# Optimization experiments

Hardware: AMD Instinct MI355X
Metric: run time of the kernel (lower is better)

## Reference

```python
import jax, jax.numpy as jnp
import numpy as np

DIM = 768
NUM_HEADS = 12
HEAD_DIM = DIM // NUM_HEADS
SCALE = HEAD_DIM ** -0.5


def setup_inputs() -> dict:
    key = jax.random.key(0)
    k1, k2, k3, k4 = jax.random.split(key, 4)
    B, N = 4, 2048
    x = jax.random.normal(k1, (B, N, DIM), dtype=jnp.float32)
    w_qkv = jax.random.normal(k2, (DIM, 3 * DIM), dtype=jnp.float32) * (DIM ** -0.5)
    w_proj = jax.random.normal(k3, (DIM, DIM), dtype=jnp.float32) * (DIM ** -0.5)
    b_proj = jax.random.normal(k4, (DIM,), dtype=jnp.float32) * 0.02
    return {"x": x, "w_qkv": w_qkv, "w_proj": w_proj, "b_proj": b_proj}


def reference(x, w_qkv, w_proj, b_proj):
    B, N, C = x.shape
    H, Dh = NUM_HEADS, HEAD_DIM
    # qkv: [B, N, 3, H, Dh] -> q,k,v each [B, H, N, Dh]
    qkv = (x @ w_qkv).reshape(B, N, 3, H, Dh)
    q = qkv[:, :, 0].transpose(0, 2, 1, 3) * SCALE
    k = qkv[:, :, 1].transpose(0, 2, 1, 3)
    v = qkv[:, :, 2].transpose(0, 2, 1, 3)
    attn = jax.nn.softmax(jnp.einsum('bhnd,bhmd->bhnm', q, k), axis=-1)
    out = jnp.einsum('bhnm,bhmd->bhnd', attn, v)  # [B, H, N, Dh]
    out = out.transpose(0, 2, 1, 3).reshape(B, N, C)
    return out @ w_proj + b_proj
```

## Files before the change

### kernel.cpp

```cpp
#include <hip/hip_runtime.h>

typedef unsigned short u16;
typedef __bf16 bf16x8 __attribute__((ext_vector_type(8)));
typedef float f32x4 __attribute__((ext_vector_type(4)));
typedef _Float16 f16x4 __attribute__((ext_vector_type(4)));
typedef unsigned short u16x8 __attribute__((ext_vector_type(8)));
typedef unsigned short u16x4 __attribute__((ext_vector_type(4)));

__device__ __forceinline__ u16 f2bf(float x) {
  union { float f; unsigned u; } c; c.f = x;
  unsigned r = c.u + 0x7FFFu + ((c.u >> 16) & 1u);
  return (u16)(r >> 16);
}

__device__ __forceinline__ void glds16(const void* g, void* s) {
  __builtin_amdgcn_global_load_lds(
      (const __attribute__((address_space(1))) unsigned int*)g,
      (__attribute__((address_space(3))) unsigned int*)s, 16, 0, 0);
}

__global__ __launch_bounds__(256) void k_pre(const float* __restrict__ x,
                                             u16* __restrict__ xbf,
                                             const float* __restrict__ wq,
                                             u16* __restrict__ wqt,
                                             const float* __restrict__ wp,
                                             u16* __restrict__ wpt) {
  __shared__ float tile[64 * 68];
  int bx = blockIdx.x;
  int tid = threadIdx.x;
  if (bx < 3072) {
    int i = bx * 256 + tid;
    const f32x4* xp = (const f32x4*)x + (size_t)i * 2;
    f32x4 a = xp[0], b = xp[1];
    u16x8 r;
    r[0] = f2bf(a[0]); r[1] = f2bf(a[1]); r[2] = f2bf(a[2]); r[3] = f2bf(a[3]);
    r[4] = f2bf(b[0]); r[5] = f2bf(b[1]); r[6] = f2bf(b[2]); r[7] = f2bf(b[3]);
    *((u16x8*)xbf + i) = r;
    return;
  }
  const float* src; u16* dst; int Nn, n0, k0;
  const int K = 768;
  if (bx < 3504) { int b2 = bx - 3072; src = wq; dst = wqt; Nn = 2304;
                   n0 = (b2 % 36) * 64; k0 = (b2 / 36) * 64; }
  else           { int b2 = bx - 3504; src = wp; dst = wpt; Nn = 768;
                   n0 = (b2 % 12) * 64; k0 = (b2 / 12) * 64; }
  int rr = tid >> 4, cc = tid & 15;
#pragma unroll
  for (int r = 0; r < 4; ++r) {
    int k = r * 16 + rr;
    f32x4 v = *(const f32x4*)(src + (size_t)(k0 + k) * Nn + n0 + cc * 4);
    *(f32x4*)(tile + k * 68 + cc * 4) = v;
  }
  __syncthreads();
#pragma unroll
  for (int r = 0; r < 4; ++r) {
    int n = r * 16 + rr;
    u16x4 o;
#pragma unroll
    for (int j = 0; j < 4; ++j) o[j] = f2bf(tile[(cc * 4 + j) * 68 + n]);
    *(u16x4*)(dst + (size_t)(n0 + n) * K + k0 + cc * 4) = o;
  }
}

template <int BM, int N, bool PROJ>
__global__ __launch_bounds__(256) void k_gemm(const u16* __restrict__ A,
                                              const u16* __restrict__ Bt,
                                              u16* __restrict__ Co,
                                              float* __restrict__ Cf,
                                              const float* __restrict__ bias,
                                              u16* __restrict__ vt) {
  const int K = 768;
  const int FI = BM / 32;
  __shared__ u16 lA[BM * 64];
  __shared__ u16 lB[128 * 64];
  const int tid = threadIdx.x;
  const int wave = tid >> 6, lane = tid & 63;
  const int lr = lane & 15, lq = lane >> 4;
  const int m0 = blockIdx.x * BM, n0 = blockIdx.y * 128;
  const int wr = (wave >> 1) * (BM / 2), wc = (wave & 1) * 64;
  f32x4 acc[FI][4] = {};
  for (int k0 = 0; k0 < K; k0 += 64) {
#pragma unroll
    for (int r = 0; r < BM / 32; ++r) {
      int ch = r * 256 + tid;
      int mm = ch >> 3, cs = ch & 7;
      glds16(A + (size_t)(m0 + mm) * K + k0 + ((cs ^ (mm & 7)) << 3), lA + ch * 8);
    }
#pragma unroll
    for (int r = 0; r < 4; ++r) {
      int ch = r * 256 + tid;
      int mm = ch >> 3, cs = ch & 7;
      glds16(Bt + (size_t)(n0 + mm) * K + k0 + ((cs ^ (mm & 7)) << 3), lB + ch * 8);
    }
    __syncthreads();
#pragma unroll
    for (int ks = 0; ks < 2; ++ks) {
      bf16x8 af[FI], bfr[4];
#pragma unroll
      for (int f = 0; f < FI; ++f) {
        int ma = wr + f * 16 + lr;
        af[f] = *(const bf16x8*)(lA + (ma * 8 + ((ks * 4 + lq) ^ (ma & 7))) * 8);
      }
#pragma unroll
      for (int f = 0; f < 4; ++f) {
        int nb = wc + f * 16 + lr;
        bfr[f] = *(const bf16x8*)(lB + (nb * 8 + ((ks * 4 + lq) ^ (nb & 7))) * 8);
      }
#pragma unroll
      for (int fi = 0; fi < FI; ++fi)
#pragma unroll
        for (int fj = 0; fj < 4; ++fj)
          acc[fi][fj] = __builtin_amdgcn_mfma_f32_16x16x32_bf16(
              af[fi], bfr[fj], acc[fi][fj], 0, 0, 0);
    }
    __syncthreads();
  }
#pragma unroll
  for (int fi = 0; fi < FI; ++fi) {
#pragma unroll
    for (int fj = 0; fj < 4; ++fj) {
      int row = m0 + wr + fi * 16 + lq * 4;
      int col = n0 + wc + fj * 16 + lr;
      if constexpr (PROJ) {
        float bv = bias[col];
#pragma unroll
        for (int g = 0; g < 4; ++g)
          Cf[(size_t)(row + g) * N + col] = acc[fi][fj][g] + bv;
      } else {
        if (n0 + wc >= 1536) {
          int hh = (col - 1536) >> 6, dd = col & 63;
          int sl = row & 2047;
          int g4 = (sl >> 2) & 31;
          int p = ((g4 >> 3) << 3) | ((g4 & 3) << 1) | ((g4 >> 2) & 1);
          int seqp = (sl & ~127) | (p << 2);
          u16x4 o;
#pragma unroll
          for (int g = 0; g < 4; ++g) o[g] = f2bf(acc[fi][fj][g]);
          *(u16x4*)(vt + (((size_t)(row >> 11) * 12 + hh) * 64 + dd) * 2048 +
                    seqp) = o;
        } else {
          const float qs = 0.18033688011112042f;
          float s = (col < 768) ? qs : 1.0f;
#pragma unroll
          for (int g = 0; g < 4; ++g)
            Co[(size_t)(row + g) * N + col] = f2bf(acc[fi][fj][g] * s);
        }
      }
    }
  }
}

__global__ __launch_bounds__(256, 2) void k_attn(const u16* __restrict__ qkv,
                                                 const u16* __restrict__ vt,
                                                 u16* __restrict__ p0,
                                                 u16* __restrict__ p1,
                                                 float* __restrict__ Lp) {
  const int SEQ = 2048, C3 = 2304;
  __shared__ u16 lds[32768];
  const int tid = threadIdx.x;
  const int wave = tid >> 6, lane = tid & 63;
  const int lr = lane & 15, lq = lane >> 4;
  const int n0 = blockIdx.x * 256;
  const int bh = blockIdx.y;
  const int jh = blockIdx.z;
  const int b = bh / 12, h = bh % 12;
  const u16* qb = qkv + (size_t)b * SEQ * C3 + h * 64;
  const u16* kb = qb + 768;
  const u16* vb = vt + (size_t)bh * 64 * SEQ;

#pragma unroll
  for (int r = 0; r < 8; ++r) {
    int ch = r * 256 + tid;
    int mm = ch >> 3, cs = ch & 7;
    glds16(qb + (size_t)(n0 + mm) * C3 + ((cs ^ (mm & 7)) << 3), lds + ch * 8);
  }
  __syncthreads();
  bf16x8 qf[4][2];
#pragma unroll
  for (int rf = 0; rf < 4; ++rf) {
    int mq = wave * 64 + rf * 16 + lr;
#pragma unroll
    for (int ks = 0; ks < 2; ++ks)
      qf[rf][ks] = *(const bf16x8*)(lds + (mq * 8 + ((ks * 4 + lq) ^ (mq & 7))) * 8);
  }
  __syncthreads();

  const f32x4 biasC = {-8.f, -8.f, -8.f, -8.f};
  union { u16x8 u; bf16x8 b; } onesU;
#pragma unroll
  for (int e = 0; e < 8; ++e) onesU.u[e] = 0x3F80;
  const bf16x8 onesA = onesU.b;
  f32x4 O[4][4] = {};
  f32x4 L5[4] = {};

  auto stage = [&](int t, int buf) {
    int j0 = jh * 1024 + t * 128;
    u16* K_ = lds + buf * 8192;
    u16* V_ = lds + 16384 + buf * 8192;
#pragma unroll
    for (int r = 0; r < 4; ++r) {
      int ch = r * 256 + tid;
      int mm = ch >> 3, cs = ch & 7;
      glds16(kb + (size_t)(j0 + mm) * C3 + ((cs ^ (mm & 7)) << 3), K_ + ch * 8);
    }
#pragma unroll
    for (int r = 0; r < 4; ++r) {
      int ch = r * 256 + tid;
      int dd = ch >> 4, ct = ch & 15;
      glds16(vb + (size_t)dd * SEQ + j0 + ((ct ^ (dd & 7)) << 3), V_ + ch * 8);
    }
  };

  stage(0, 0);
  for (int t = 0; t < 8; ++t) {
    const int cur = t & 1;
    const u16* K_ = lds + cur * 8192;
    const u16* V_ = lds + 16384 + cur * 8192;
    asm volatile("s_barrier" ::: "memory");
    if (t < 7) {
      stage(t + 1, cur ^ 1);
      asm volatile("s_waitcnt vmcnt(8)" ::: "memory");
    } else {
      asm volatile("s_waitcnt vmcnt(0)" ::: "memory");
    }
    asm volatile("s_barrier" ::: "memory");

#pragma unroll
    for (int c = 0; c < 4; ++c) {
      f32x4 S[2][4];
#pragma unroll
      for (int j2 = 0; j2 < 2; ++j2) {
        int j = (c * 2 + j2) * 16 + lr;
        bf16x8 kf = *(const bf16x8*)(K_ + (j * 8 + (lq ^ (j & 7))) * 8);
#pragma unroll
        for (int rf = 0; rf < 4; ++rf)
          S[j2][rf] = __builtin_amdgcn_mfma_f32_16x16x32_bf16(
              kf, qf[rf][0], biasC, 0, 0, 0);
      }
#pragma unroll
      for (int j2 = 0; j2 < 2; ++j2) {
        int j = (c * 2 + j2) * 16 + lr;
        bf16x8 kf = *(const bf16x8*)(K_ + (j * 8 + ((4 + lq) ^ (j & 7))) * 8);
#pragma unroll
        for (int rf = 0; rf < 4; ++rf)
          S[j2][rf] = __builtin_amdgcn_mfma_f32_16x16x32_bf16(
              kf, qf[rf][1], S[j2][rf], 0, 0, 0);
      }
      bf16x8 P[4];
#pragma unroll
      for (int rf = 0; rf < 4; ++rf) {
        bf16x8 p8;
#pragma unroll
        for (int j2 = 0; j2 < 2; ++j2)
#pragma unroll
          for (int g = 0; g < 4; ++g)
            p8[j2 * 4 + g] = (__bf16)__builtin_amdgcn_exp2f(S[j2][rf][g]);
        P[rf] = p8;
        L5[rf] = __builtin_amdgcn_mfma_f32_16x16x32_bf16(
            onesA, P[rf], L5[rf], 0, 0, 0);
      }
#pragma unroll
      for (int df = 0; df < 4; ++df) {
        int d = df * 16 + lr;
        bf16x8 vf = *(const bf16x8*)(V_ + d * 128 + (((c * 4 + lq) ^ (d & 7)) << 3));
#pragma unroll
        for (int rf = 0; rf < 4; ++rf)
          O[rf][df] = __builtin_amdgcn_mfma_f32_16x16x32_bf16(
              vf, P[rf], O[rf][df], 0, 0, 0);
      }
    }
  }

  u16* pd = jh ? p1 : p0;
  float* Lb = Lp + (size_t)(jh * 48 + bh) * 2048;
#pragma unroll
  for (int rf = 0; rf < 4; ++rf) {
    int rowl = n0 + wave * 64 + rf * 16 + lr;
    if (lq == 0) Lb[rowl] = L5[rf][0];
    size_t row = (size_t)b * SEQ + rowl;
#pragma unroll
    for (int df = 0; df < 4; ++df) {
      union { f16x4 h; u16x4 u; } o;
#pragma unroll
      for (int g = 0; g < 4; ++g) o.h[g] = (_Float16)O[rf][df][g];
      *(u16x4*)(pd + row * 768 + h * 64 + df * 16 + lq * 4) = o.u;
    }
  }
}

__global__ __launch_bounds__(256) void k_merge(const u16* __restrict__ p0,
                                               u16* __restrict__ p1,
                                               const float* __restrict__ Lp) {
  int t = blockIdx.x * 256 + threadIdx.x;
  int row = t / 192, c4 = (t % 192) * 4;
  int hh = c4 >> 6;
  int bh = (row >> 11) * 12 + hh, rowl = row & 2047;
  float l = Lp[(size_t)bh * 2048 + rowl] + Lp[(size_t)(48 + bh) * 2048 + rowl];
  float inv = 1.0f / l;
  size_t off = (size_t)row * 768 + c4;
  union { f16x4 h; u16x4 u; } a, bb;
  a.u = *(const u16x4*)(p0 + off);
  bb.u = *(const u16x4*)(p1 + off);
  u16x4 o;
#pragma unroll
  for (int g = 0; g < 4; ++g)
    o[g] = f2bf(((float)a.h[g] + (float)bb.h[g]) * inv);
  *(u16x4*)(p1 + off) = o;
}

extern "C" void kernel_launch(void* const* d_in, const int* in_sizes, int n_in,
                              void* d_out, int out_size, void* d_ws, size_t ws_size,
                              hipStream_t stream) {
  const float* x = (const float*)d_in[0];
  const float* w_qkv = (const float*)d_in[1];
  const float* w_proj = (const float*)d_in[2];
  const float* b_proj = (const float*)d_in[3];
  float* out = (float*)d_out;
  char* ws = (char*)d_ws;
  u16* x_bf    = (u16*)(ws);
  u16* wqkv_t  = (u16*)(ws + 12582912);
  u16* wproj_t = (u16*)(ws + 16121856);
  u16* qkv     = (u16*)(ws + 17301504);
  u16* vt      = (u16*)(ws + 55050240);
  u16* aout    = (u16*)(ws + 67633152);
  float* Lp    = (float*)wqkv_t;

  k_pre<<<3648, 256, 0, stream>>>(x, x_bf, w_qkv, wqkv_t, w_proj, wproj_t);
  k_gemm<128, 2304, false><<<dim3(64, 18), 256, 0, stream>>>(x_bf, wqkv_t, qkv,
                                                             nullptr, nullptr, vt);
  k_attn<<<dim3(8, 48, 2), 256, 0, stream>>>(qkv, vt, x_bf, aout, Lp);
  k_merge<<<6144, 256, 0, stream>>>(x_bf, aout, Lp);
  k_gemm<64, 768, true><<<dim3(128, 6), 256, 0, stream>>>(aout, wproj_t, nullptr,
                                                          out, b_proj, nullptr);
}
```

Baseline: 215.9 us.

## Double-buffer GEMM K-loop and single-buffer V in attention for higher occupancy

The QKV/proj GEMM kernel now walks K in 32-wide steps with double-buffered LDS, issuing the next tile's async global-to-LDS loads while the current tile runs MFMAs, and declares 4 blocks per CU. The attention kernel keeps K double-buffered but gives V a single buffer, loaded each iteration and waited on only after the first QK chunk. This cuts attention LDS enough to target 3 blocks per CU. The aim is better latency hiding and occupancy, at the cost of more barriers per K-step and a tighter register budget under the new launch bounds.

```diff
diff --git a/kernel.cpp b/kernel.cpp
--- a/kernel.cpp
+++ b/kernel.cpp
@@ -63,58 +63,78 @@
 }
 
 template <int BM, int N, bool PROJ>
-__global__ __launch_bounds__(256) void k_gemm(const u16* __restrict__ A,
-                                              const u16* __restrict__ Bt,
-                                              u16* __restrict__ Co,
-                                              float* __restrict__ Cf,
-                                              const float* __restrict__ bias,
-                                              u16* __restrict__ vt) {
+__global__ __launch_bounds__(256, 4) void k_gemm(const u16* __restrict__ A,
+                                                 const u16* __restrict__ Bt,
+                                                 u16* __restrict__ Co,
+                                                 float* __restrict__ Cf,
+                                                 const float* __restrict__ bias,
+                                                 u16* __restrict__ vt) {
   const int K = 768;
   const int FI = BM / 32;
-  __shared__ u16 lA[BM * 64];
-  __shared__ u16 lB[128 * 64];
+  __shared__ u16 lds[2 * (BM + 128) * 32];
   const int tid = threadIdx.x;
   const int wave = tid >> 6, lane = tid & 63;
   const int lr = lane & 15, lq = lane >> 4;
   const int m0 = blockIdx.x * BM, n0 = blockIdx.y * 128;
   const int wr = (wave >> 1) * (BM / 2), wc = (wave & 1) * 64;
   f32x4 acc[FI][4] = {};
-  for (int k0 = 0; k0 < K; k0 += 64) {
-#pragma unroll
-    for (int r = 0; r < BM / 32; ++r) {
+
+  auto stage = [&](int t, int buf) {
+    int k0 = t * 32;
+    u16* sA = lds + buf * ((BM + 128) * 32);
+    u16* sB = sA + BM * 32;
+#pragma unroll
+    for (int r = 0; r < BM / 64; ++r) {
       int ch = r * 256 + tid;
-      int mm = ch >> 3, cs = ch & 7;
-      glds16(A + (size_t)(m0 + mm) * K + k0 + ((cs ^ (mm & 7)) << 3), lA + ch * 8);
-    }
-#pragma unroll
-    for (int r = 0; r < 4; ++r) {
+      int mm = ch >> 2, cs = ch & 3;
+      glds16(A + (size_t)(m0 + mm) * K + k0 + ((cs ^ ((mm >> 1) & 3)) << 3),
+             sA + ch * 8);
+    }
+#pragma unroll
+    for (int r = 0; r < 2; ++r) {
       int ch = r * 256 + tid;
-      int mm = ch >> 3, cs = ch & 7;
-      glds16(Bt + (size_t)(n0 + mm) * K + k0 + ((cs ^ (mm & 7)) << 3), lB + ch * 8);
-    }
-    __syncthreads();
-#pragma unroll
-    for (int ks = 0; ks < 2; ++ks) {
-      bf16x8 af[FI], bfr[4];
-#pragma unroll
-      for (int f = 0; f < FI; ++f) {
-        int ma = wr + f * 16 + lr;
-        af[f] = *(const bf16x8*)(lA + (ma * 8 + ((ks * 4 + lq) ^ (ma & 7))) * 8);
-      }
-#pragma unroll
-      for (int f = 0; f < 4; ++f) {
-        int nb = wc + f * 16 + lr;
-        bfr[f] = *(const bf16x8*)(lB + (nb * 8 + ((ks * 4 + lq) ^ (nb & 7))) * 8);
-      }
-#pragma unroll
-      for (int fi = 0; fi < FI; ++fi)
-#pragma unroll
-        for (int fj = 0; fj < 4; ++fj)
-          acc[fi][fj] = __builtin_amdgcn_mfma_f32_16x16x32_bf16(
-              af[fi], bfr[fj], acc[fi][fj], 0, 0, 0);
-    }
-    __syncthreads();
-  }
+      int mm = ch >> 2, cs = ch & 3;
+      glds16(Bt + (size_t)(n0 + mm) * K + k0 + ((cs ^ ((mm >> 1) & 3)) << 3),
+             sB + ch * 8);
+    }
+  };
+
+  stage(0, 0);
+  for (int t = 0; t < 24; ++t) {
+    const int cur = t & 1;
+    const u16* sA = lds + cur * ((BM + 128) * 32);
+    const u16* sB = sA + BM * 32;
+    asm volatile("s_barrier" ::: "memory");
+    if (t < 23) {
+      stage(t + 1, cur ^ 1);
+      if constexpr (BM == 128)
+        asm volatile("s_waitcnt vmcnt(4)" ::: "memory");
+      else
+        asm volatile("s_waitcnt vmcnt(3)" ::: "memory");
+    } else {
+      asm volatile("s_waitcnt vmcnt(0)" ::: "memory");
+    }
+    asm volatile("s_barrier" ::: "memory");
+
+    bf16x8 af[FI], bfr[4];
+#pragma unroll
+    for (int f = 0; f < FI; ++f) {
+      int ma = wr + f * 16 + lr;
+      af[f] = *(const bf16x8*)(sA + ma * 32 + ((lq ^ ((ma >> 1) & 3)) << 3));
+    }
+#pragma unroll
+    for (int f = 0; f < 4; ++f) {
+      int nb = wc + f * 16 + lr;
+      bfr[f] = *(const bf16x8*)(sB + nb * 32 + ((lq ^ ((nb >> 1) & 3)) << 3));
+    }
+#pragma unroll
+    for (int fi = 0; fi < FI; ++fi)
+#pragma unroll
+      for (int fj = 0; fj < 4; ++fj)
+        acc[fi][fj] = __builtin_amdgcn_mfma_f32_16x16x32_bf16(
+            af[fi], bfr[fj], acc[fi][fj], 0, 0, 0);
+  }
+
 #pragma unroll
   for (int fi = 0; fi < FI; ++fi) {
 #pragma unroll
@@ -150,13 +170,13 @@
   }
 }
 
-__global__ __launch_bounds__(256, 2) void k_attn(const u16* __restrict__ qkv,
+__global__ __launch_bounds__(256, 3) void k_attn(const u16* __restrict__ qkv,
                                                  const u16* __restrict__ vt,
                                                  u16* __restrict__ p0,
                                                  u16* __restrict__ p1,
                                                  float* __restrict__ Lp) {
   const int SEQ = 2048, C3 = 2304;
-  __shared__ u16 lds[32768];
+  __shared__ u16 lds[24576];
   const int tid = threadIdx.x;
   const int wave = tid >> 6, lane = tid & 63;
   const int lr = lane & 15, lq = lane >> 4;
@@ -193,16 +213,19 @@
   f32x4 O[4][4] = {};
   f32x4 L5[4] = {};
 
-  auto stage = [&](int t, int buf) {
+  auto stageK = [&](int t, int buf) {
     int j0 = jh * 1024 + t * 128;
     u16* K_ = lds + buf * 8192;
-    u16* V_ = lds + 16384 + buf * 8192;
 #pragma unroll
     for (int r = 0; r < 4; ++r) {
       int ch = r * 256 + tid;
       int mm = ch >> 3, cs = ch & 7;
       glds16(kb + (size_t)(j0 + mm) * C3 + ((cs ^ (mm & 7)) << 3), K_ + ch * 8);
     }
+  };
+  auto stageV = [&](int t) {
+    int j0 = jh * 1024 + t * 128;
+    u16* V_ = lds + 16384;
 #pragma unroll
     for (int r = 0; r < 4; ++r) {
       int ch = r * 256 + tid;
@@ -211,63 +234,78 @@
     }
   };
 
-  stage(0, 0);
+  bf16x8 P[4];
+  auto qk_chunk = [&](int c, const u16* K_) {
+    f32x4 S[2][4];
+#pragma unroll
+    for (int j2 = 0; j2 < 2; ++j2) {
+      int j = (c * 2 + j2) * 16 + lr;
+      bf16x8 kf = *(const bf16x8*)(K_ + (j * 8 + (lq ^ (j & 7))) * 8);
+#pragma unroll
+      for (int rf = 0; rf < 4; ++rf)
+        S[j2][rf] = __builtin_amdgcn_mfma_f32_16x16x32_bf16(
+            kf, qf[rf][0], biasC, 0, 0, 0);
+    }
+#pragma unroll
+    for (int j2 = 0; j2 < 2; ++j2) {
+      int j = (c * 2 + j2) * 16 + lr;
+      bf16x8 kf = *(const bf16x8*)(K_ + (j * 8 + ((4 + lq) ^ (j & 7))) * 8);
+#pragma unroll
+      for (int rf = 0; rf < 4; ++rf)
+        S[j2][rf] = __builtin_amdgcn_mfma_f32_16x16x32_bf16(
+            kf, qf[rf][1], S[j2][rf], 0, 0, 0);
+    }
+#pragma unroll
+    for (int rf = 0; rf < 4; ++rf) {
+      bf16x8 p8;
+#pragma unroll
+      for (int j2 = 0; j2 < 2; ++j2)
+#pragma unroll
+        for (int g = 0; g < 4; ++g)
+          p8[j2 * 4 + g] = (__bf16)__builtin_amdgcn_exp2f(S[j2][rf][g]);
+      P[rf] = p8;
+      L5[rf] = __builtin_amdgcn_mfma_f32_16x16x32_bf16(onesA, P[rf], L5[rf],
+                                                       0, 0, 0);
+    }
+  };
+  auto pv_chunk = [&](int c, const u16* V_) {
+#pragma unroll
+    for (int df = 0; df < 4; ++df) {
+      int d = df * 16 + lr;
+      bf16x8 vf = *(const bf16x8*)(V_ + d * 128 + (((c * 4 + lq) ^ (d & 7)) << 3));
+#pragma unroll
+      for (int rf = 0; rf < 4; ++rf)
+        O[rf][df] = __builtin_amdgcn_mfma_f32_16x16x32_bf16(
+            vf, P[rf], O[rf][df], 0, 0, 0);
+    }
+  };
+
+  stageK(0, 0);
   for (int t = 0; t < 8; ++t) {
     const int cur = t & 1;
     const u16* K_ = lds + cur * 8192;
-    const u16* V_ = lds + 16384 + cur * 8192;
-    asm volatile("s_barrier" ::: "memory");
+    const u16* V_ = lds + 16384;
+    asm volatile("s_barrier" ::: "memory");
+    stageV(t);
     if (t < 7) {
-      stage(t + 1, cur ^ 1);
+      stageK(t + 1, cur ^ 1);
       asm volatile("s_waitcnt vmcnt(8)" ::: "memory");
     } else {
+      asm volatile("s_waitcnt vmcnt(4)" ::: "memory");
+    }
+    asm volatile("s_barrier" ::: "memory");
+
+    qk_chunk(0, K_);
+    if (t < 7)
+      asm volatile("s_waitcnt vmcnt(4)" ::: "memory");
+    else
       asm volatile("s_waitcnt vmcnt(0)" ::: "memory");
-    }
-    asm volatile("s_barrier" ::: "memory");
-
-#pragma unroll
-    for (int c = 0; c < 4; ++c) {
-      f32x4 S[2][4];
-#pragma unroll
-      for (int j2 = 0; j2 < 2; ++j2) {
-        int j = (c * 2 + j2) * 16 + lr;
-        bf16x8 kf = *(const bf16x8*)(K_ + (j * 8 + (lq ^ (j & 7))) * 8);
-#pragma unroll
-        for (int rf = 0; rf < 4; ++rf)
-          S[j2][rf] = __builtin_amdgcn_mfma_f32_16x16x32_bf16(
-              kf, qf[rf][0], biasC, 0, 0, 0);
-      }
-#pragma unroll
-      for (int j2 = 0; j2 < 2; ++j2) {
-        int j = (c * 2 + j2) * 16 + lr;
-        bf16x8 kf = *(const bf16x8*)(K_ + (j * 8 + ((4 + lq) ^ (j & 7))) * 8);
-#pragma unroll
-        for (int rf = 0; rf < 4; ++rf)
-          S[j2][rf] = __builtin_amdgcn_mfma_f32_16x16x32_bf16(
-              kf, qf[rf][1], S[j2][rf], 0, 0, 0);
-      }
-      bf16x8 P[4];
-#pragma unroll
-      for (int rf = 0; rf < 4; ++rf) {
-        bf16x8 p8;
-#pragma unroll
-        for (int j2 = 0; j2 < 2; ++j2)
-#pragma unroll
-          for (int g = 0; g < 4; ++g)
-            p8[j2 * 4 + g] = (__bf16)__builtin_amdgcn_exp2f(S[j2][rf][g]);
-        P[rf] = p8;
-        L5[rf] = __builtin_amdgcn_mfma_f32_16x16x32_bf16(
-            onesA, P[rf], L5[rf], 0, 0, 0);
-      }
-#pragma unroll
-      for (int df = 0; df < 4; ++df) {
-        int d = df * 16 + lr;
-        bf16x8 vf = *(const bf16x8*)(V_ + d * 128 + (((c * 4 + lq) ^ (d & 7)) << 3));
-#pragma unroll
-        for (int rf = 0; rf < 4; ++rf)
-          O[rf][df] = __builtin_amdgcn_mfma_f32_16x16x32_bf16(
-              vf, P[rf], O[rf][df], 0, 0, 0);
-      }
+    asm volatile("s_barrier" ::: "memory");
+    pv_chunk(0, V_);
+#pragma unroll
+    for (int c = 1; c < 4; ++c) {
+      qk_chunk(c, K_);
+      pv_chunk(c, V_);
     }
   }
 
```

New measurement: 327.7 us. 1.52x slower.
